# Kernel optimization log

Hardware: AMD Instinct MI355X
Metric: run time of the kernel (lower is better)

The kernel has to match this reference:

```python
import jax, jax.numpy as jnp
import numpy as np

N, E, G, D, L = 20000, 320000, 256, 256, 5
EPS = 1e-5


def _bn(h, g, b):
    # BatchNorm1d in training mode: biased batch statistics over the row dim
    m = h.mean(axis=0)
    v = jnp.mean((h - m) ** 2, axis=0)
    return g * (h - m) / jnp.sqrt(v + EPS) + b


def setup_inputs() -> dict:
    key = jax.random.key(0)
    ks = iter(jax.random.split(key, 40))

    def rn(shape, s=0.1):
        return jax.random.normal(next(ks), shape, dtype=jnp.float32) * s

    inp = {}
    inp['x_feats'] = jax.random.randint(next(ks), (N, 6), 0, 4)
    inp['edge_index'] = jax.random.randint(next(ks), (2, E), 0, N)
    inp['edge_attr'] = jax.random.randint(next(ks), (E, 5), 0, 2)
    inp['batch'] = jnp.sort(jax.random.randint(next(ks), (N,), 0, G))
    inp['nt1'] = rn((119, D)); inp['nt2'] = rn((4, D)); inp['nt3'] = rn((7, D))
    inp['nt4'] = rn((8, D)); inp['nt5'] = rn((5, D)); inp['nt6'] = rn((7, D))
    inp['et1'] = rn((L, 5, D)); inp['et2'] = rn((L, 4, D)); inp['et3'] = rn((L, 2, D))
    inp['et4'] = rn((L, 2, D)); inp['et5'] = rn((L, 2, D))
    inp['w1'] = rn((L, 2 * D, D)); inp['b1'] = rn((L, 2 * D))
    inp['w2'] = rn((L, D, 2 * D)); inp['b2'] = rn((L, D))
    inp['bng'] = 1.0 + rn((L, D)); inp['bnb'] = rn((L, D))
    inp['pw'] = rn((3, D, D)); inp['pg'] = 1.0 + rn((3, D)); inp['pb'] = rn((3, D))
    inp['ow1'] = rn((D // 2, D)); inp['ob1'] = rn((D // 2,))
    inp['ow2'] = rn((2, D // 2)); inp['ob2'] = rn((2,))
    return inp


def reference(x_feats, edge_index, edge_attr, batch,
              nt1, nt2, nt3, nt4, nt5, nt6,
              et1, et2, et3, et4, et5,
              w1, b1, w2, b2, bng, bnb,
              pw, pg, pb, ow1, ob1, ow2, ob2):
    n = x_feats.shape[0]
    # atom embedding: sum of 6 feature embeddings -> [N, D]
    h = (nt1[x_feats[:, 0]] + nt2[x_feats[:, 1]] + nt3[x_feats[:, 2]]
         + nt4[x_feats[:, 3]] + nt5[x_feats[:, 4]] + nt6[x_feats[:, 5]])
    src, dst = edge_index[0], edge_index[1]
    for l in range(L):
        # edge embedding for real edges: [E, D]
        e = (et1[l][edge_attr[:, 0]] + et2[l][edge_attr[:, 1]] + et3[l][edge_attr[:, 2]]
             + et4[l][edge_attr[:, 3]] + et5[l][edge_attr[:, 4]])
        # self-loop edges carry attr [4,0,0,0,0]
        self_e = et1[l][4] + et2[l][0] + et3[l][0] + et4[l][0] + et5[l][0]
        # message = x_j + e, scatter-add into destinations; self loops add h + self_e
        aggr = jax.ops.segment_sum(h[src] + e, dst, num_segments=n) + h + self_e
        # GIN MLP update: D -> 2D -> D
        hh = jax.nn.relu(aggr @ w1[l].T + b1[l]) @ w2[l].T + b2[l]
        # batchnorm then relu (dropout=0; the layer==num_layer branch is unreachable)
        h = jax.nn.relu(_bn(hh, bng[l], bnb[l]))
    # global mean pool over graphs
    counts = jax.ops.segment_sum(jnp.ones((n, 1), h.dtype), batch, num_segments=G)
    hg = jax.ops.segment_sum(h, batch, num_segments=G) / jnp.maximum(counts, 1.0)
    # proj head: (Linear no-bias, BN, ReLU) x2, then Linear no-bias + BN
    for i in range(3):
        hg = _bn(hg @ pw[i].T, pg[i], pb[i])
        if i < 2:
            hg = jax.nn.relu(hg)
    # output MLP: Linear -> Softplus -> Linear
    return jax.nn.softplus(hg @ ow1.T + ob1) @ ow2.T + ob2
```

## Files before the change

### kernel.cpp

```cpp
#include <hip/hip_runtime.h>

#define DD 256
#define TWO_D 512
#define NLAYER 5
#define NGRAPH 256
#define BNEPS 1e-5f

typedef __attribute__((ext_vector_type(8))) _Float16 half8;
typedef __attribute__((ext_vector_type(4))) _Float16 half4;
typedef __attribute__((ext_vector_type(4))) float f32x4;

#define MFMA16 __builtin_amdgcn_mfma_f32_16x16x32_f16

__global__ __launch_bounds__(256) void prep_kernel(
    const int* __restrict__ xf,
    const float* __restrict__ nt1, const float* __restrict__ nt2,
    const float* __restrict__ nt3, const float* __restrict__ nt4,
    const float* __restrict__ nt5, const float* __restrict__ nt6,
    _Float16* __restrict__ h16,
    const float* __restrict__ w1, const float* __restrict__ w2,
    _Float16* __restrict__ w1f, _Float16* __restrict__ w2f,
    const float* __restrict__ et1, const float* __restrict__ et2,
    const float* __restrict__ et3, const float* __restrict__ et4,
    const float* __restrict__ et5, _Float16* __restrict__ etab,
    int* __restrict__ deg, int* __restrict__ zr, int zr_words,
    const int* __restrict__ ei, const int* __restrict__ ea,
    int* __restrict__ packed,
    int N, int E)
{
  const int t = threadIdx.x;
  const int b = blockIdx.x;
  const int B_EMB = N;
  const int B_WC  = 128;
  const int B_ET  = NLAYER * 33;
  const int B_ZR  = 96;

  if (b < B_EMB) {
    int i = b, j = t;
    int x0 = xf[i*6+0], x1 = xf[i*6+1], x2 = xf[i*6+2];
    int x3 = xf[i*6+3], x4 = xf[i*6+4], x5 = xf[i*6+5];
    float v = nt1[x0*DD+j] + nt2[x1*DD+j] + nt3[x2*DD+j]
            + nt4[x3*DD+j] + nt5[x4*DD+j] + nt6[x5*DD+j];
    h16[(size_t)i*DD + j] = (_Float16)v;
  } else if (b < B_EMB + B_WC) {
    int bid = b - B_EMB;
    int n = NLAYER * TWO_D * DD;
    for (int i = bid*256 + t; i < n; i += B_WC*256) {
      int l = i >> 17, rem = i & 131071;
      int r = rem >> 8, k = rem & 255;
      int o1 = (l<<17) + (((r>>4)<<3) + (k>>5))*512 + ((((k>>3)&3)<<4) + (r&15))*8 + (k&7);
      w1f[o1] = (_Float16)w1[i];
      int r2 = rem >> 9, k2 = rem & 511;
      int o2 = (l<<17) + (((r2>>4)<<4) + (k2>>5))*512 + ((((k2>>3)&3)<<4) + (r2&15))*8 + (k2&7);
      w2f[o2] = (_Float16)w2[i];
    }
  } else if (b < B_EMB + B_WC + B_ET) {
    int bid = b - B_EMB - B_WC;
    int l = bid / 33, c = bid % 33;
    int j = t;
    int a0 = (c==32)?4:(c&1);
    int a1 = (c==32)?0:((c>>1)&1);
    int a2 = (c==32)?0:((c>>2)&1);
    int a3 = (c==32)?0:((c>>3)&1);
    int a4 = (c==32)?0:((c>>4)&1);
    etab[((size_t)l*33 + c)*DD + j] = (_Float16)(
        et1[(l*5+a0)*DD+j] + et2[(l*4+a1)*DD+j] + et3[(l*2+a2)*DD+j]
      + et4[(l*2+a3)*DD+j] + et5[(l*2+a4)*DD+j]);
  } else if (b < B_EMB + B_WC + B_ET + B_ZR) {
    int bid = b - B_EMB - B_WC - B_ET;
    int tw = N + zr_words;
    for (int i = bid*256 + t; i < tw; i += B_ZR*256) {
      if (i < N) deg[i] = 0;
      else zr[i - N] = 0;
    }
  } else {
    int bid = b - B_EMB - B_WC - B_ET - B_ZR;
    int e = bid*256 + t;
    if (e < E) {
      int src = ei[e];
      int code = (ea[e*5+0]&1) | ((ea[e*5+1]&1)<<1) | ((ea[e*5+2]&1)<<2)
               | ((ea[e*5+3]&1)<<3) | ((ea[e*5+4]&1)<<4);
      packed[e] = src | (code << 16);
    }
  }
}

__global__ __launch_bounds__(256) void hist_kernel(
    const int* __restrict__ ei, int* __restrict__ deg, int E)
{
  int e = blockIdx.x*256 + threadIdx.x;
  if (e < E) atomicAdd(&deg[ei[E + e]], 1);
}

__global__ __launch_bounds__(1024) void scan_kernel(
    const int* __restrict__ deg, int* __restrict__ row_start,
    int* __restrict__ cursor, int N)
{
  __shared__ int sh[1024];
  int t = threadIdx.x;
  const int CH = (N + 1023) >> 10;
  int base = t * CH;
  int lim = N - base; if (lim < 0) lim = 0; if (lim > CH) lim = CH;
  int s = 0;
  for (int i = 0; i < lim; ++i) s += deg[base + i];
  sh[t] = s;
  __syncthreads();
  for (int off = 1; off < 1024; off <<= 1) {
    int x = (t >= off) ? sh[t - off] : 0;
    __syncthreads();
    sh[t] += x;
    __syncthreads();
  }
  int run = t ? sh[t-1] : 0;
  for (int i = 0; i < lim; ++i) {
    row_start[base+i] = run; cursor[base+i] = run;
    run += deg[base+i];
  }
  if (t == 1023) row_start[N] = sh[1023];
}

__global__ __launch_bounds__(256) void scatter_kernel(
    const int* __restrict__ ei, const int* __restrict__ packed,
    int* __restrict__ cursor, int* __restrict__ esort, int E)
{
  int e = blockIdx.x*256 + threadIdx.x;
  if (e >= E) return;
  int dst = ei[E + e];
  int pos = atomicAdd(&cursor[dst], 1);
  esort[pos] = packed[e];
}

template<int APPLY_BN>
__global__ __launch_bounds__(256) void aggr_kernel(
    const _Float16* __restrict__ hsrc, const _Float16* __restrict__ etab_l,
    const int* __restrict__ row_start, const int* __restrict__ esort,
    const float* __restrict__ stats_prev, const float* __restrict__ g,
    const float* __restrict__ bb, float inv_n,
    _Float16* __restrict__ aggrh, int N)
{
  __shared__ __attribute__((aligned(16))) _Float16 se[33*DD];
  for (int i = threadIdx.x; i < 33*DD/8; i += 256)
    ((int4*)se)[i] = ((const int4*)etab_l)[i];
  __syncthreads();
  const int wave = threadIdx.x >> 6, lane = threadIdx.x & 63;
  const int c4 = lane << 2;
  float sc0=1.f, sc1=1.f, sc2=1.f, sc3=1.f, sh0=0.f, sh1=0.f, sh2=0.f, sh3=0.f;
  if (APPLY_BN) {
#define MKSC(k, SC, SH) { float m_ = stats_prev[c4+k]*inv_n;                      \
    float v_ = fmaxf(stats_prev[DD+c4+k]*inv_n - m_*m_, 0.f);                     \
    SC = g[c4+k]*rsqrtf(v_+BNEPS); SH = bb[c4+k] - m_*SC; }
    MKSC(0, sc0, sh0) MKSC(1, sc1, sh1) MKSC(2, sc2, sh2) MKSC(3, sc3, sh3)
#undef MKSC
  }
  const int W0 = blockIdx.x*4 + wave, NW = gridDim.x*4;

#define BNX(h4, o0, o1, o2, o3)                                           \
  { float t0_ = (float)(h4).x, t1_ = (float)(h4).y,                       \
          t2_ = (float)(h4).z, t3_ = (float)(h4).w;                       \
    if (APPLY_BN) {                                                       \
      t0_ = fmaxf(t0_*sc0 + sh0, 0.f); t1_ = fmaxf(t1_*sc1 + sh1, 0.f);  \
      t2_ = fmaxf(t2_*sc2 + sh2, 0.f); t3_ = fmaxf(t3_*sc3 + sh3, 0.f);  \
    }                                                                     \
    o0 = t0_; o1 = t1_; o2 = t2_; o3 = t3_; }

  for (int node = W0; node < N; node += NW) {
    int p  = row_start[node];
    int pe = row_start[node+1];
    const half4 hv = *(const half4*)(hsrc + (size_t)node*DD + c4);
    const half4 sv = *(const half4*)(se + 32*DD + c4);
    float ax, ay, az, aw;
    BNX(hv, ax, ay, az, aw);
    ax += (float)sv.x; ay += (float)sv.y; az += (float)sv.z; aw += (float)sv.w;
    for (; p + 4 <= pe; p += 4) {
      int pk0 = esort[p], pk1 = esort[p+1], pk2 = esort[p+2], pk3 = esort[p+3];
      const half4 h0 = *(const half4*)(hsrc + (size_t)(pk0 & 0xffff)*DD + c4);
      const half4 h1 = *(const half4*)(hsrc + (size_t)(pk1 & 0xffff)*DD + c4);
      const half4 h2 = *(const half4*)(hsrc + (size_t)(pk2 & 0xffff)*DD + c4);
      const half4 h3 = *(const half4*)(hsrc + (size_t)(pk3 & 0xffff)*DD + c4);
      const half4 e0 = *(const half4*)(se + (pk0 >> 16)*DD + c4);
      const half4 e1 = *(const half4*)(se + (pk1 >> 16)*DD + c4);
      const half4 e2 = *(const half4*)(se + (pk2 >> 16)*DD + c4);
      const half4 e3 = *(const half4*)(se + (pk3 >> 16)*DD + c4);
      float b0x,b0y,b0z,b0w, b1x,b1y,b1z,b1w, b2x,b2y,b2z,b2w, b3x,b3y,b3z,b3w;
      BNX(h0, b0x,b0y,b0z,b0w); BNX(h1, b1x,b1y,b1z,b1w);
      BNX(h2, b2x,b2y,b2z,b2w); BNX(h3, b3x,b3y,b3z,b3w);
      ax += (b0x+(float)e0.x) + (b1x+(float)e1.x) + (b2x+(float)e2.x) + (b3x+(float)e3.x);
      ay += (b0y+(float)e0.y) + (b1y+(float)e1.y) + (b2y+(float)e2.y) + (b3y+(float)e3.y);
      az += (b0z+(float)e0.z) + (b1z+(float)e1.z) + (b2z+(float)e2.z) + (b3z+(float)e3.z);
      aw += (b0w+(float)e0.w) + (b1w+(float)e1.w) + (b2w+(float)e2.w) + (b3w+(float)e3.w);
    }
    for (; p < pe; ++p) {
      int pk = esort[p];
      const half4 hx = *(const half4*)(hsrc + (size_t)(pk & 0xffff)*DD + c4);
      const half4 ex = *(const half4*)(se + (pk >> 16)*DD + c4);
      float bx, by, bz, bw;
      BNX(hx, bx, by, bz, bw);
      ax += bx + (float)ex.x; ay += by + (float)ex.y;
      az += bz + (float)ex.z; aw += bw + (float)ex.w;
    }
    half4 o;
    o.x = (_Float16)ax; o.y = (_Float16)ay; o.z = (_Float16)az; o.w = (_Float16)aw;
    *(half4*)(aggrh + (size_t)node*DD + c4) = o;
  }
#undef BNX
}

__global__ __launch_bounds__(512) void mlp_kernel(
    const _Float16* __restrict__ A,
    const _Float16* __restrict__ W1f,
    const float* __restrict__ b1,
    const _Float16* __restrict__ W2f,
    const float* __restrict__ b2,
    _Float16* __restrict__ O,
    float* __restrict__ stats,
    int Nreal)
{
  __shared__ __attribute__((aligned(16))) _Float16 sA[32*256];
  __shared__ __attribute__((aligned(16))) _Float16 sH[32*128];
  const int m0 = blockIdx.x << 5;
  const int t = threadIdx.x;
  const int w = t >> 6, lane = t & 63;
  const int r15 = lane & 15, quad = lane >> 4;
  const int rx = r15 & 7;

#pragma unroll
  for (int i = 0; i < 2; ++i) {
    int seg = (i << 9) + t;
    int row = seg >> 5, s = seg & 31;
    half8 v = *(const half8*)(A + (size_t)(m0 + row)*DD + (s << 3));
    *(half8*)(sA + (row << 8) + ((s ^ (row & 7)) << 3)) = v;
  }
  __syncthreads();

  f32x4 acc2[2][2] = {};
#pragma unroll 1
  for (int c = 0; c < 4; ++c) {
    f32x4 acc1[2] = {};
    const _Float16* W1b = W1f + (((c << 3) + w) << 12);
#pragma unroll
    for (int ks = 0; ks < 8; ++ks) {
      int so = (((ks << 2) + quad) ^ rx) << 3;
      half8 a0 = *(const half8*)(sA + (r15 << 8) + so);
      half8 a1 = *(const half8*)(sA + ((16 + r15) << 8) + so);
      half8 bf = *(const half8*)(W1b + (ks << 9) + (lane << 3));
      acc1[0] = MFMA16(a0, bf, acc1[0], 0, 0, 0);
      acc1[1] = MFMA16(a1, bf, acc1[1], 0, 0, 0);
    }
    {
      int colL = (w << 4) + r15;
      float bv = b1[(c << 7) + colL];
#pragma unroll
      for (int fm = 0; fm < 2; ++fm)
#pragma unroll
        for (int r = 0; r < 4; ++r) {
          int row = (fm << 4) + (quad << 2) + r;
          float v = fmaxf(acc1[fm][r] + bv, 0.f);
          sH[(row << 7) + ((((colL >> 3) ^ (row & 7)) << 3)) + (colL & 7)] = (_Float16)v;
        }
    }
    __syncthreads();
#pragma unroll
    for (int ks = 0; ks < 4; ++ks) {
      int so = (((ks << 2) + quad) ^ rx) << 3;
      half8 a0 = *(const half8*)(sH + (r15 << 7) + so);
      half8 a1 = *(const half8*)(sH + ((16 + r15) << 7) + so);
      int ks2 = (c << 2) + ks;
      half8 b0 = *(const half8*)(W2f + ((((w << 1) + 0) << 13)) + (ks2 << 9) + (lane << 3));
      half8 b1v = *(const half8*)(W2f + ((((w << 1) + 1) << 13)) + (ks2 << 9) + (lane << 3));
      acc2[0][0] = MFMA16(a0, b0, acc2[0][0], 0, 0, 0);
      acc2[0][1] = MFMA16(a0, b1v, acc2[0][1], 0, 0, 0);
      acc2[1][0] = MFMA16(a1, b0, acc2[1][0], 0, 0, 0);
      acc2[1][1] = MFMA16(a1, b1v, acc2[1][1], 0, 0, 0);
    }
    __syncthreads();
  }

#pragma unroll
  for (int fn = 0; fn < 2; ++fn) {
    int col = (w << 5) + (fn << 4) + r15;
    float bv = b2[col];
    float s1 = 0.f, s2 = 0.f;
#pragma unroll
    for (int fm = 0; fm < 2; ++fm)
#pragma unroll
      for (int r = 0; r < 4; ++r) {
        int row = (fm << 4) + (quad << 2) + r;
        float v = acc2[fm][fn][r] + bv;
        sA[(row << 8) + (((col >> 3) ^ (row & 7)) << 3) + (col & 7)] = (_Float16)v;
        if (m0 + row < Nreal) { s1 += v; s2 += v*v; }
      }
    s1 += __shfl_xor(s1, 16); s1 += __shfl_xor(s1, 32);
    s2 += __shfl_xor(s2, 16); s2 += __shfl_xor(s2, 32);
    if (lane < 16) { atomicAdd(&stats[col], s1); atomicAdd(&stats[DD + col], s2); }
  }
  __syncthreads();
#pragma unroll
  for (int i = 0; i < 2; ++i) {
    int seg = (i << 9) + t;
    int row = seg >> 5, s = seg & 31;
    half8 v = *(const half8*)(sA + (row << 8) + ((s ^ (row & 7)) << 3));
    *(half8*)(O + (size_t)(m0 + row)*DD + (s << 3)) = v;
  }
}

__global__ __launch_bounds__(256) void pool_kernel(
    const _Float16* __restrict__ hh16, const float* __restrict__ stats_prev,
    const float* __restrict__ g, const float* __restrict__ bb, float inv_n,
    const int* __restrict__ batch,
    float* __restrict__ hgsum, int* __restrict__ hgcnt, int N)
{
  int j = threadIdx.x;
  float m = stats_prev[j]*inv_n;
  float var = fmaxf(stats_prev[DD+j]*inv_n - m*m, 0.f);
  float sc = g[j]*rsqrtf(var + BNEPS);
  float sh = bb[j] - m*sc;
  int r0 = blockIdx.x * 64;
  int cur = -1; float acc = 0.f; int run = 0;
  for (int r = 0; r < 64; ++r) {
    int row = r0 + r;
    if (row >= N) break;
    int gg = batch[row];
    if (gg != cur) {
      if (cur >= 0) {
        atomicAdd(&hgsum[(size_t)cur*DD + j], acc);
        if (j == 0) atomicAdd(&hgcnt[cur], run);
      }
      cur = gg; acc = 0.f; run = 0;
    }
    float v = (float)hh16[(size_t)row*DD + j];
    acc += fmaxf(v*sc + sh, 0.f);
    run++;
  }
  if (cur >= 0) {
    atomicAdd(&hgsum[(size_t)cur*DD + j], acc);
    if (j == 0) atomicAdd(&hgcnt[cur], run);
  }
}

template<int MODE>
__global__ __launch_bounds__(256) void proj_gemm_kernel(
    const float* __restrict__ in, const int* __restrict__ cnt,
    const float* __restrict__ pstat_prev,
    const float* __restrict__ gprev, const float* __restrict__ bprev,
    const float* __restrict__ W,
    float* __restrict__ outb, float* __restrict__ pstat)
{
  __shared__ float sA[16][17];
  __shared__ float sB[16][17];
  int tx = threadIdx.x, ty = threadIdx.y;
  int r = blockIdx.y*16 + ty;
  int c = blockIdx.x*16 + tx;
  float acc = 0.f;
  for (int k0 = 0; k0 < DD; k0 += 16) {
    int k = k0 + tx;
    float a = in[(size_t)r*DD + k];
    if (MODE == 0) {
      a /= (float)max(cnt[r], 1);
    } else {
      float m = pstat_prev[k] * (1.0f/NGRAPH);
      float var = fmaxf(pstat_prev[DD + k] * (1.0f/NGRAPH) - m*m, 0.f);
      float sc = gprev[k] * rsqrtf(var + BNEPS);
      a = fmaxf((a - m)*sc + bprev[k], 0.f);
    }
    sA[ty][tx] = a;
    sB[ty][tx] = W[(size_t)(blockIdx.x*16 + ty)*DD + k0 + tx];
    __syncthreads();
#pragma unroll
    for (int kk = 0; kk < 16; ++kk) acc += sA[ty][kk] * sB[tx][kk];
    __syncthreads();
  }
  outb[(size_t)r*DD + c] = acc;
  sA[ty][tx] = acc; sB[ty][tx] = acc*acc;
  __syncthreads();
  for (int o = 8; o > 0; o >>= 1) {
    if (ty < o) { sA[ty][tx] += sA[ty+o][tx]; sB[ty][tx] += sB[ty+o][tx]; }
    __syncthreads();
  }
  if (ty == 0) { atomicAdd(&pstat[c], sA[0][tx]); atomicAdd(&pstat[DD + c], sB[0][tx]); }
}

__global__ __launch_bounds__(128) void out_kernel(
    const float* __restrict__ t2, const float* __restrict__ pstat2,
    const float* __restrict__ g2, const float* __restrict__ b2p,
    const float* __restrict__ ow1, const float* __restrict__ ob1,
    const float* __restrict__ ow2, const float* __restrict__ ob2,
    float* __restrict__ outp)
{
  __shared__ float rowv[DD];
  __shared__ float z[128];
  int r = blockIdx.x, t = threadIdx.x;
#pragma unroll
  for (int half = 0; half < 2; ++half) {
    int j = t + half*128;
    float m = pstat2[j] * (1.0f/NGRAPH);
    float var = fmaxf(pstat2[DD + j] * (1.0f/NGRAPH) - m*m, 0.f);
    float sc = g2[j] * rsqrtf(var + BNEPS);
    rowv[j] = (t2[(size_t)r*DD + j] - m)*sc + b2p[j];
  }
  __syncthreads();
  float a = ob1[t];
  for (int k = 0; k < DD; ++k) a += rowv[k] * ow1[(size_t)t*DD + k];
  z[t] = fmaxf(a, 0.f) + log1pf(expf(-fabsf(a)));
  __syncthreads();
  if (t < 2) {
    float o = ob2[t];
    for (int k = 0; k < 128; ++k) o += z[k] * ow2[t*128 + k];
    outp[r*2 + t] = o;
  }
}

extern "C" void kernel_launch(void* const* d_in, const int* in_sizes, int n_in,
                              void* d_out, int out_size, void* d_ws, size_t ws_size,
                              hipStream_t stream)
{
  const int* x_feats = (const int*)d_in[0];
  const int* ei      = (const int*)d_in[1];
  const int* ea      = (const int*)d_in[2];
  const int* batch   = (const int*)d_in[3];
  const float* nt1 = (const float*)d_in[4];
  const float* nt2 = (const float*)d_in[5];
  const float* nt3 = (const float*)d_in[6];
  const float* nt4 = (const float*)d_in[7];
  const float* nt5 = (const float*)d_in[8];
  const float* nt6 = (const float*)d_in[9];
  const float* et1 = (const float*)d_in[10];
  const float* et2 = (const float*)d_in[11];
  const float* et3 = (const float*)d_in[12];
  const float* et4 = (const float*)d_in[13];
  const float* et5 = (const float*)d_in[14];
  const float* w1  = (const float*)d_in[15];
  const float* b1  = (const float*)d_in[16];
  const float* w2  = (const float*)d_in[17];
  const float* b2  = (const float*)d_in[18];
  const float* bng = (const float*)d_in[19];
  const float* bnb = (const float*)d_in[20];
  const float* pw  = (const float*)d_in[21];
  const float* pg  = (const float*)d_in[22];
  const float* pb  = (const float*)d_in[23];
  const float* ow1 = (const float*)d_in[24];
  const float* ob1 = (const float*)d_in[25];
  const float* ow2 = (const float*)d_in[26];
  const float* ob2 = (const float*)d_in[27];

  const int N = in_sizes[0] / 6;
  const int E = in_sizes[1] / 2;
  const int Mp = ((N + 31) >> 5) << 5;

  unsigned char* wp = (unsigned char*)d_ws;
  size_t off = 0;
  auto carve = [&](size_t bytes) -> void* {
    void* p = wp + off;
    off += (bytes + 255) & ~(size_t)255;
    return p;
  };

  _Float16* h16      = (_Float16*)carve((size_t)N * DD * 2);
  _Float16* aggrh    = (_Float16*)carve((size_t)Mp * DD * 2);
  _Float16* hh16     = (_Float16*)carve((size_t)Mp * DD * 2);
  _Float16* w1f      = (_Float16*)carve((size_t)NLAYER * TWO_D * DD * 2);
  _Float16* w2f      = (_Float16*)carve((size_t)NLAYER * TWO_D * DD * 2);
  _Float16* etabg    = (_Float16*)carve((size_t)NLAYER * 33 * DD * 2);
  int* deg           = (int*)carve((size_t)N * 4);
  int* row_start     = (int*)carve((size_t)(N + 1) * 4);
  int* cursor        = (int*)carve((size_t)N * 4);
  int* packed        = (int*)carve((size_t)E * 4);
  int* esort         = (int*)carve((size_t)E * 4);
  float* stats       = (float*)carve((size_t)NLAYER * 2 * DD * 4);
  float* hgsum       = (float*)carve((size_t)NGRAPH * DD * 4);
  int* hgcnt         = (int*)carve((size_t)NGRAPH * 4);
  float* pstats      = (float*)carve(3 * 2 * DD * 4);
  const int ZR_WORDS = NLAYER*2*DD + NGRAPH*DD + NGRAPH + 3*2*DD;
  float* hgA         = (float*)carve((size_t)NGRAPH * DD * 4);
  float* hgB         = (float*)carve((size_t)NGRAPH * DD * 4);
  float* t0c         = (float*)carve((size_t)NGRAPH * DD * 4);
  (void)ws_size; (void)n_in; (void)out_size;

  const int EB = (E + 255) / 256;
  const float inv_n = 1.0f / (float)N;

  const int PREP_BLOCKS = N + 128 + NLAYER*33 + 96 + EB;
  prep_kernel<<<PREP_BLOCKS, 256, 0, stream>>>(
      x_feats, nt1, nt2, nt3, nt4, nt5, nt6, h16,
      w1, w2, w1f, w2f,
      et1, et2, et3, et4, et5, etabg,
      deg, (int*)stats, ZR_WORDS,
      ei, ea, packed, N, E);
  hist_kernel<<<EB, 256, 0, stream>>>(ei, deg, E);
  scan_kernel<<<1, 1024, 0, stream>>>(deg, row_start, cursor, N);
  scatter_kernel<<<EB, 256, 0, stream>>>(ei, packed, cursor, esort, E);

  const int MB = Mp >> 5;
  for (int l = 0; l < NLAYER; ++l) {
    float* st_prev = stats + (size_t)(l-1)*2*DD;
    float* st_cur  = stats + (size_t)l*2*DD;
    if (l == 0) {
      aggr_kernel<0><<<2048, 256, 0, stream>>>(h16, etabg, row_start, esort,
                                               nullptr, nullptr, nullptr, inv_n,
                                               aggrh, N);
    } else {
      aggr_kernel<1><<<2048, 256, 0, stream>>>(hh16, etabg + (size_t)l*33*DD,
                                               row_start, esort,
                                               st_prev, bng + (l-1)*DD, bnb + (l-1)*DD,
                                               inv_n, aggrh, N);
    }
    mlp_kernel<<<MB, 512, 0, stream>>>(
        aggrh, w1f + ((size_t)l << 17), b1 + l*TWO_D,
        w2f + ((size_t)l << 17), b2 + l*DD,
        hh16, st_cur, N);
  }

  pool_kernel<<<(N + 63) / 64, 256, 0, stream>>>(
      hh16, stats + (size_t)(NLAYER-1)*2*DD, bng + (NLAYER-1)*DD, bnb + (NLAYER-1)*DD,
      inv_n, batch, hgsum, hgcnt, N);

  dim3 pgrid(16, 16), pblk(16, 16);
  proj_gemm_kernel<0><<<pgrid, pblk, 0, stream>>>(
      hgsum, hgcnt, nullptr, nullptr, nullptr,
      pw + 0*DD*DD, hgA, pstats + 0*2*DD);
  proj_gemm_kernel<1><<<pgrid, pblk, 0, stream>>>(
      hgA, nullptr, pstats + 0*2*DD, pg + 0*DD, pb + 0*DD,
      pw + 1*DD*DD, hgB, pstats + 1*2*DD);
  proj_gemm_kernel<1><<<pgrid, pblk, 0, stream>>>(
      hgB, nullptr, pstats + 1*2*DD, pg + 1*DD, pb + 1*DD,
      pw + 2*DD*DD, t0c, pstats + 2*2*DD);
  out_kernel<<<NGRAPH, 128, 0, stream>>>(
      t0c, pstats + 2*2*DD, pg + 2*DD, pb + 2*DD,
      ow1, ob1, ow2, ob2, (float*)d_out);
}
```

Before: 558.7 us.

## Double MLP row tile to 64, unroll aggregation by 8, shrink pool chunks

The MLP kernel now processes 64 rows per block instead of 32, so each weight fragment loaded from global memory feeds four MFMA row tiles instead of two. This halves total weight traffic, at the cost of more LDS and more accumulator registers; a launch-bounds occupancy hint is added to compensate. The aggregation gather loop is unrolled to 8 edges so more independent loads are in flight. The pool kernel uses 16-row chunks, giving more blocks and more parallelism.

```diff
diff --git a/kernel.cpp b/kernel.cpp
--- a/kernel.cpp
+++ b/kernel.cpp
@@ -162,6 +162,11 @@
       t2_ = fmaxf(t2_*sc2 + sh2, 0.f); t3_ = fmaxf(t3_*sc3 + sh3, 0.f);  \
     }                                                                     \
     o0 = t0_; o1 = t1_; o2 = t2_; o3 = t3_; }
+#define ACC4(hx, ex)                                                      \
+  { float bx_, by_, bz_, bw_;                                             \
+    BNX(hx, bx_, by_, bz_, bw_);                                          \
+    ax += bx_ + (float)(ex).x; ay += by_ + (float)(ex).y;                 \
+    az += bz_ + (float)(ex).z; aw += bw_ + (float)(ex).w; }
 
   for (int node = W0; node < N; node += NW) {
     int p  = row_start[node];
@@ -171,41 +176,55 @@
     float ax, ay, az, aw;
     BNX(hv, ax, ay, az, aw);
     ax += (float)sv.x; ay += (float)sv.y; az += (float)sv.z; aw += (float)sv.w;
-    for (; p + 4 <= pe; p += 4) {
-      int pk0 = esort[p], pk1 = esort[p+1], pk2 = esort[p+2], pk3 = esort[p+3];
-      const half4 h0 = *(const half4*)(hsrc + (size_t)(pk0 & 0xffff)*DD + c4);
-      const half4 h1 = *(const half4*)(hsrc + (size_t)(pk1 & 0xffff)*DD + c4);
-      const half4 h2 = *(const half4*)(hsrc + (size_t)(pk2 & 0xffff)*DD + c4);
-      const half4 h3 = *(const half4*)(hsrc + (size_t)(pk3 & 0xffff)*DD + c4);
+    for (; p + 8 <= pe; p += 8) {
+      int pk0 = esort[p],   pk1 = esort[p+1], pk2 = esort[p+2], pk3 = esort[p+3];
+      int pk4 = esort[p+4], pk5 = esort[p+5], pk6 = esort[p+6], pk7 = esort[p+7];
+      const half4 a0 = *(const half4*)(hsrc + (size_t)(pk0 & 0xffff)*DD + c4);
+      const half4 a1 = *(const half4*)(hsrc + (size_t)(pk1 & 0xffff)*DD + c4);
+      const half4 a2 = *(const half4*)(hsrc + (size_t)(pk2 & 0xffff)*DD + c4);
+      const half4 a3 = *(const half4*)(hsrc + (size_t)(pk3 & 0xffff)*DD + c4);
+      const half4 a4 = *(const half4*)(hsrc + (size_t)(pk4 & 0xffff)*DD + c4);
+      const half4 a5 = *(const half4*)(hsrc + (size_t)(pk5 & 0xffff)*DD + c4);
+      const half4 a6 = *(const half4*)(hsrc + (size_t)(pk6 & 0xffff)*DD + c4);
+      const half4 a7 = *(const half4*)(hsrc + (size_t)(pk7 & 0xffff)*DD + c4);
       const half4 e0 = *(const half4*)(se + (pk0 >> 16)*DD + c4);
       const half4 e1 = *(const half4*)(se + (pk1 >> 16)*DD + c4);
       const half4 e2 = *(const half4*)(se + (pk2 >> 16)*DD + c4);
       const half4 e3 = *(const half4*)(se + (pk3 >> 16)*DD + c4);
-      float b0x,b0y,b0z,b0w, b1x,b1y,b1z,b1w, b2x,b2y,b2z,b2w, b3x,b3y,b3z,b3w;
-      BNX(h0, b0x,b0y,b0z,b0w); BNX(h1, b1x,b1y,b1z,b1w);
-      BNX(h2, b2x,b2y,b2z,b2w); BNX(h3, b3x,b3y,b3z,b3w);
-      ax += (b0x+(float)e0.x) + (b1x+(float)e1.x) + (b2x+(float)e2.x) + (b3x+(float)e3.x);
-      ay += (b0y+(float)e0.y) + (b1y+(float)e1.y) + (b2y+(float)e2.y) + (b3y+(float)e3.y);
-      az += (b0z+(float)e0.z) + (b1z+(float)e1.z) + (b2z+(float)e2.z) + (b3z+(float)e3.z);
-      aw += (b0w+(float)e0.w) + (b1w+(float)e1.w) + (b2w+(float)e2.w) + (b3w+(float)e3.w);
+      const half4 e4 = *(const half4*)(se + (pk4 >> 16)*DD + c4);
+      const half4 e5 = *(const half4*)(se + (pk5 >> 16)*DD + c4);
+      const half4 e6 = *(const half4*)(se + (pk6 >> 16)*DD + c4);
+      const half4 e7 = *(const half4*)(se + (pk7 >> 16)*DD + c4);
+      ACC4(a0, e0) ACC4(a1, e1) ACC4(a2, e2) ACC4(a3, e3)
+      ACC4(a4, e4) ACC4(a5, e5) ACC4(a6, e6) ACC4(a7, e7)
+    }
+    for (; p + 4 <= pe; p += 4) {
+      int pk0 = esort[p], pk1 = esort[p+1], pk2 = esort[p+2], pk3 = esort[p+3];
+      const half4 a0 = *(const half4*)(hsrc + (size_t)(pk0 & 0xffff)*DD + c4);
+      const half4 a1 = *(const half4*)(hsrc + (size_t)(pk1 & 0xffff)*DD + c4);
+      const half4 a2 = *(const half4*)(hsrc + (size_t)(pk2 & 0xffff)*DD + c4);
+      const half4 a3 = *(const half4*)(hsrc + (size_t)(pk3 & 0xffff)*DD + c4);
+      const half4 e0 = *(const half4*)(se + (pk0 >> 16)*DD + c4);
+      const half4 e1 = *(const half4*)(se + (pk1 >> 16)*DD + c4);
+      const half4 e2 = *(const half4*)(se + (pk2 >> 16)*DD + c4);
+      const half4 e3 = *(const half4*)(se + (pk3 >> 16)*DD + c4);
+      ACC4(a0, e0) ACC4(a1, e1) ACC4(a2, e2) ACC4(a3, e3)
     }
     for (; p < pe; ++p) {
       int pk = esort[p];
       const half4 hx = *(const half4*)(hsrc + (size_t)(pk & 0xffff)*DD + c4);
       const half4 ex = *(const half4*)(se + (pk >> 16)*DD + c4);
-      float bx, by, bz, bw;
-      BNX(hx, bx, by, bz, bw);
-      ax += bx + (float)ex.x; ay += by + (float)ex.y;
-      az += bz + (float)ex.z; aw += bw + (float)ex.w;
+      ACC4(hx, ex)
     }
     half4 o;
     o.x = (_Float16)ax; o.y = (_Float16)ay; o.z = (_Float16)az; o.w = (_Float16)aw;
     *(half4*)(aggrh + (size_t)node*DD + c4) = o;
   }
+#undef ACC4
 #undef BNX
 }
 
-__global__ __launch_bounds__(512) void mlp_kernel(
+__global__ __launch_bounds__(512, 3) void mlp_kernel(
     const _Float16* __restrict__ A,
     const _Float16* __restrict__ W1f,
     const float* __restrict__ b1,
@@ -215,16 +234,16 @@
     float* __restrict__ stats,
     int Nreal)
 {
-  __shared__ __attribute__((aligned(16))) _Float16 sA[32*256];
-  __shared__ __attribute__((aligned(16))) _Float16 sH[32*128];
-  const int m0 = blockIdx.x << 5;
+  __shared__ __attribute__((aligned(16))) _Float16 sA[64*256];
+  __shared__ __attribute__((aligned(16))) _Float16 sH[64*128];
+  const int m0 = blockIdx.x << 6;
   const int t = threadIdx.x;
   const int w = t >> 6, lane = t & 63;
   const int r15 = lane & 15, quad = lane >> 4;
   const int rx = r15 & 7;
 
 #pragma unroll
-  for (int i = 0; i < 2; ++i) {
+  for (int i = 0; i < 4; ++i) {
     int seg = (i << 9) + t;
     int row = seg >> 5, s = seg & 31;
     half8 v = *(const half8*)(A + (size_t)(m0 + row)*DD + (s << 3));
@@ -232,45 +251,46 @@
   }
   __syncthreads();
 
-  f32x4 acc2[2][2] = {};
+  f32x4 acc2[4][2] = {};
 #pragma unroll 1
   for (int c = 0; c < 4; ++c) {
-    f32x4 acc1[2] = {};
+    f32x4 acc1[4] = {};
     const _Float16* W1b = W1f + (((c << 3) + w) << 12);
 #pragma unroll
     for (int ks = 0; ks < 8; ++ks) {
       int so = (((ks << 2) + quad) ^ rx) << 3;
-      half8 a0 = *(const half8*)(sA + (r15 << 8) + so);
-      half8 a1 = *(const half8*)(sA + ((16 + r15) << 8) + so);
       half8 bf = *(const half8*)(W1b + (ks << 9) + (lane << 3));
-      acc1[0] = MFMA16(a0, bf, acc1[0], 0, 0, 0);
-      acc1[1] = MFMA16(a1, bf, acc1[1], 0, 0, 0);
+#pragma unroll
+      for (int fm = 0; fm < 4; ++fm) {
+        half8 af = *(const half8*)(sA + (((fm << 4) + r15) << 8) + so);
+        acc1[fm] = MFMA16(af, bf, acc1[fm], 0, 0, 0);
+      }
     }
     {
       int colL = (w << 4) + r15;
       float bv = b1[(c << 7) + colL];
-#pragma unroll
-      for (int fm = 0; fm < 2; ++fm)
+      int cs = colL >> 3;
+#pragma unroll
+      for (int fm = 0; fm < 4; ++fm)
 #pragma unroll
         for (int r = 0; r < 4; ++r) {
           int row = (fm << 4) + (quad << 2) + r;
           float v = fmaxf(acc1[fm][r] + bv, 0.f);
-          sH[(row << 7) + ((((colL >> 3) ^ (row & 7)) << 3)) + (colL & 7)] = (_Float16)v;
+          sH[(row << 7) + ((cs ^ (row & 7)) << 3) + (colL & 7)] = (_Float16)v;
         }
     }
     __syncthreads();
 #pragma unroll
     for (int ks = 0; ks < 4; ++ks) {
       int so = (((ks << 2) + quad) ^ rx) << 3;
-      half8 a0 = *(const half8*)(sH + (r15 << 7) + so);
-      half8 a1 = *(const half8*)(sH + ((16 + r15) << 7) + so);
-      int ks2 = (c << 2) + ks;
-      half8 b0 = *(const half8*)(W2f + ((((w << 1) + 0) << 13)) + (ks2 << 9) + (lane << 3));
-      half8 b1v = *(const half8*)(W2f + ((((w << 1) + 1) << 13)) + (ks2 << 9) + (lane << 3));
-      acc2[0][0] = MFMA16(a0, b0, acc2[0][0], 0, 0, 0);
-      acc2[0][1] = MFMA16(a0, b1v, acc2[0][1], 0, 0, 0);
-      acc2[1][0] = MFMA16(a1, b0, acc2[1][0], 0, 0, 0);
-      acc2[1][1] = MFMA16(a1, b1v, acc2[1][1], 0, 0, 0);
+      half8 b0  = *(const half8*)(W2f + (((w << 1) + 0) << 13) + (((c << 2) + ks) << 9) + (lane << 3));
+      half8 b1v = *(const half8*)(W2f + (((w << 1) + 1) << 13) + (((c << 2) + ks) << 9) + (lane << 3));
+#pragma unroll
+      for (int fm = 0; fm < 4; ++fm) {
+        half8 af = *(const half8*)(sH + (((fm << 4) + r15) << 7) + so);
+        acc2[fm][0] = MFMA16(af, b0,  acc2[fm][0], 0, 0, 0);
+        acc2[fm][1] = MFMA16(af, b1v, acc2[fm][1], 0, 0, 0);
+      }
     }
     __syncthreads();
   }
@@ -281,7 +301,7 @@
     float bv = b2[col];
     float s1 = 0.f, s2 = 0.f;
 #pragma unroll
-    for (int fm = 0; fm < 2; ++fm)
+    for (int fm = 0; fm < 4; ++fm)
 #pragma unroll
       for (int r = 0; r < 4; ++r) {
         int row = (fm << 4) + (quad << 2) + r;
@@ -295,7 +315,7 @@
   }
   __syncthreads();
 #pragma unroll
-  for (int i = 0; i < 2; ++i) {
+  for (int i = 0; i < 4; ++i) {
     int seg = (i << 9) + t;
     int row = seg >> 5, s = seg & 31;
     half8 v = *(const half8*)(sA + (row << 8) + ((s ^ (row & 7)) << 3));
@@ -314,9 +334,9 @@
   float var = fmaxf(stats_prev[DD+j]*inv_n - m*m, 0.f);
   float sc = g[j]*rsqrtf(var + BNEPS);
   float sh = bb[j] - m*sc;
-  int r0 = blockIdx.x * 64;
+  int r0 = blockIdx.x * 16;
   int cur = -1; float acc = 0.f; int run = 0;
-  for (int r = 0; r < 64; ++r) {
+  for (int r = 0; r < 16; ++r) {
     int row = r0 + r;
     if (row >= N) break;
     int gg = batch[row];
@@ -444,7 +464,7 @@
 
   const int N = in_sizes[0] / 6;
   const int E = in_sizes[1] / 2;
-  const int Mp = ((N + 31) >> 5) << 5;
+  const int Mp = ((N + 63) >> 6) << 6;
 
   unsigned char* wp = (unsigned char*)d_ws;
   size_t off = 0;
@@ -489,7 +509,7 @@
   scan_kernel<<<1, 1024, 0, stream>>>(deg, row_start, cursor, N);
   scatter_kernel<<<EB, 256, 0, stream>>>(ei, packed, cursor, esort, E);
 
-  const int MB = Mp >> 5;
+  const int MB = Mp >> 6;
   for (int l = 0; l < NLAYER; ++l) {
     float* st_prev = stats + (size_t)(l-1)*2*DD;
     float* st_cur  = stats + (size_t)l*2*DD;
@@ -509,7 +529,7 @@
         hh16, st_cur, N);
   }
 
-  pool_kernel<<<(N + 63) / 64, 256, 0, stream>>>(
+  pool_kernel<<<(N + 15) / 16, 256, 0, stream>>>(
       hh16, stats + (size_t)(NLAYER-1)*2*DD, bng + (NLAYER-1)*DD, bnb + (NLAYER-1)*DD,
       inv_n, batch, hgsum, hgcnt, N);
 
```

Result: no change. 566.1 us (+1.3%).
